# Kernel optimization log

Measured on AMD Instinct MI355X. Metric: run time of the kernel, lower is better.

## Reference

```python
import jax, jax.numpy as jnp
import numpy as np

B = 8192       # number of windows (batch*windows_per_image)
N = 49         # tokens per 7x7 window
C = 128        # channels
H = 4          # heads
HD = C // H    # head dim = 32
WIN = (7, 7)


def _relative_position_index(win):
    wh, ww = win
    coords = np.stack(np.meshgrid(np.arange(wh), np.arange(ww), indexing='ij'))
    cf = coords.reshape(2, -1)                       # (2, N)
    rel = (cf[:, :, None] - cf[:, None, :]).transpose(1, 2, 0)  # (N, N, 2)
    rel[:, :, 0] += wh - 1
    rel[:, :, 1] += ww - 1
    rel[:, :, 0] *= 2 * ww - 1
    return jnp.array(rel.sum(-1).reshape(-1), dtype=jnp.int32)  # (N*N,)


def setup_inputs() -> dict:
    key = jax.random.key(0)
    ks = jax.random.split(key, 7)
    x = jax.random.normal(ks[0], (B, N, C), dtype=jnp.float32)
    mask = jax.random.normal(ks[1], (B, 1, N, N), dtype=jnp.float32)
    qkv_w = jax.random.normal(ks[2], (C, 3 * C), dtype=jnp.float32) * (C ** -0.5)
    qkv_b = jnp.zeros((3 * C,), dtype=jnp.float32)
    rel_bias_table = jax.random.normal(ks[3], ((2 * WIN[0] - 1) * (2 * WIN[1] - 1), H), dtype=jnp.float32)
    proj_w = jax.random.normal(ks[4], (C, C), dtype=jnp.float32) * (C ** -0.5)
    proj_b = jnp.zeros((C,), dtype=jnp.float32)
    rel_index = _relative_position_index(WIN)
    return {"x": x, "mask": mask, "qkv_w": qkv_w, "qkv_b": qkv_b,
            "rel_bias_table": rel_bias_table, "proj_w": proj_w,
            "proj_b": proj_b, "rel_index": rel_index}


def reference(x, mask, qkv_w, qkv_b, rel_bias_table, proj_w, proj_b, rel_index):
    b, n, c = x.shape
    scale = HD ** -0.5
    qkv = (x @ qkv_w + qkv_b).reshape(b, n, 3, H, HD).transpose(2, 0, 3, 1, 4)
    q, k, v = qkv[0] * scale, qkv[1], qkv[2]          # (b, H, n, HD)
    attn = jnp.einsum('bhqd,bhkd->bhqk', q, k)        # (b, H, n, n)
    # gathered relative position bias: (n*n, H) -> (1, H, n, n)
    bias = rel_bias_table[rel_index].reshape(n, n, H).transpose(2, 0, 1)[None]
    attn = jax.nn.softmax(attn + bias + mask, axis=-1)
    out = jnp.einsum('bhqk,bhkd->bhqd', attn, v)       # (b, H, n, HD)
    out = out.transpose(0, 2, 1, 3).reshape(b, n, c)
    return out @ proj_w + proj_b
```

## Files before the change

### kernel.cpp

```cpp
#include <hip/hip_runtime.h>
#include <hip/hip_bf16.h>

using f32x4 = __attribute__((ext_vector_type(4))) float;
using bf16x8 = __attribute__((ext_vector_type(8))) short;

#define DEVI __device__ __forceinline__

DEVI short f2bf(float f) { __hip_bfloat16 h = __float2bfloat16(f); return *reinterpret_cast<short*>(&h); }
DEVI unsigned int pk2(float a, float b) {
    float2 t; t.x = a; t.y = b;
    __hip_bfloat162 h = __float22bfloat162_rn(t);
    return *reinterpret_cast<unsigned int*>(&h);
}
DEVI float bf2f(unsigned short s) { unsigned int u = ((unsigned int)s) << 16; return __uint_as_float(u); }

DEVI void pl32swap(unsigned& a, unsigned& b) { asm("v_permlane32_swap_b32 %0, %1" : "+v"(a), "+v"(b)); }
DEVI void pl16swap(unsigned& a, unsigned& b) { asm("v_permlane16_swap_b32 %0, %1" : "+v"(a), "+v"(b)); }

#define GLOAD_LDS16(gp, lp) \
    __builtin_amdgcn_global_load_lds((const __attribute__((address_space(1))) void*)(gp), \
                                     (__attribute__((address_space(3))) void*)(lp), 16, 0, 0)

constexpr int NB = 8192;
constexpr int NT = 49;
constexpr int CD = 128;
constexpr float SCALE = 0.17677669529663687f;
constexpr float LOG2E = 1.4426950408889634f;

constexpr size_t WS_QKVWT  = 0;
constexpr size_t WS_PROJWT = 98304;
constexpr size_t WS_BIAS   = 131072;

DEVI void div49(unsigned grow, unsigned& bI, unsigned& tI) {
    bI = (unsigned)(((unsigned long long)grow * 2804876602ull) >> 37);
    tI = grow - bI * 49u;
}

DEVI int swz128(int row, int col) { return row * 128 + (col ^ ((row & 7) << 3)); }

__global__ __launch_bounds__(256) void prep_kernel(
    const float* __restrict__ qkv_w, const float* __restrict__ proj_w,
    const float* __restrict__ rbt, const int* __restrict__ rel_index,
    short* __restrict__ qkvwS, short* __restrict__ projwT, unsigned short* __restrict__ biasBf)
{
    int i = blockIdx.x * 256 + threadIdx.x;
    if (i < 384 * 128) {
        int n = i >> 7, j = i & 127;
        int c = n >> 7, r = n & 127;
        qkvwS[c * 16384 + r * 128 + (j ^ ((r & 7) << 3))] = f2bf(qkv_w[j * 384 + n]);
    }
    if (i < 128 * 128) {
        int n = i >> 7, j = i & 127;
        projwT[n * 128 + j] = f2bf(proj_w[j * 128 + n]);
    }
    if (i < 4 * NT * NT) {
        int h = i / (NT * NT); int t = i % (NT * NT);
        int k = t / NT, q = t - k * NT;
        biasBf[i] = (unsigned short)f2bf(rbt[rel_index[q * NT + k] * 4 + h] * LOG2E);
    }
}

__global__ __launch_bounds__(512, 4) void fused_kernel(
    const float* __restrict__ x, const float* __restrict__ mask,
    const float* __restrict__ qkv_b, const short* __restrict__ qkvwS,
    const unsigned short* __restrict__ biasT, const short* __restrict__ projwT,
    const float* __restrict__ proj_b, float* __restrict__ out)
{
    __shared__ __attribute__((aligned(16))) short pool[40960];
    short* qkL = pool;
    short* vS  = pool + 16384;
    char*  Wcb = (char*)(pool + 24576);
    float* mT  = (float*)(pool + 24576);

    const int b = blockIdx.x;
    const int tid = threadIdx.x;
    const int w = tid >> 6, lane = tid & 63, lr = lane & 15, lg = lane >> 4;
    const int h = w >> 1, half = w & 1;

    const float* mb_ = mask + (size_t)b * (NT * NT);
    float mreg[5];
#pragma unroll
    for (int ii = 0; ii < 5; ++ii) {
        int i = tid + ii * 512;
        mreg[ii] = (i < NT * NT) ? mb_[i] * LOG2E : 0.f;
    }

    bf16x8 af[2][4];
#pragma unroll
    for (int mf = 0; mf < 2; ++mf) {
        const int row = 32 * (w & 1) + 16 * mf + lr;
        const bool valid = row < NT;
        const float* xrow = x + ((size_t)b * NT + (valid ? row : 0)) * CD;
#pragma unroll
        for (int kt = 0; kt < 4; ++kt) {
            float4 v0 = {0.f,0.f,0.f,0.f}, v1 = {0.f,0.f,0.f,0.f};
            if (valid) {
                const float4* p = reinterpret_cast<const float4*>(xrow + kt * 32 + lg * 8);
                v0 = p[0]; v1 = p[1];
            }
            union { unsigned int u[4]; bf16x8 v; } cv;
            cv.u[0] = pk2(v0.x, v0.y); cv.u[1] = pk2(v0.z, v0.w);
            cv.u[2] = pk2(v1.x, v1.y); cv.u[3] = pk2(v1.z, v1.w);
            af[mf][kt] = cv.v;
        }
    }

    float biasr[3][2];
#pragma unroll
    for (int c = 0; c < 3; ++c)
#pragma unroll
        for (int nn = 0; nn < 2; ++nn)
            biasr[c][nn] = qkv_b[(c * 8 + (w >> 1) + 4 * nn) * 16 + lr];

    const char* srcW = (const char*)qkvwS;
#pragma unroll
    for (int c = 0; c < 3; ++c) {
#pragma unroll
        for (int i = 0; i < 4; ++i)
            GLOAD_LDS16(srcW + c * 32768 + w * 4096 + i * 1024 + lane * 16,
                        Wcb + w * 4096 + i * 1024);
        __syncthreads();

#pragma unroll
        for (int nn = 0; nn < 2; ++nn) {
            const int ntl = (w >> 1) + 4 * nn;
            const int nt  = c * 8 + ntl;
            const int s   = nt >> 3;
            const int hh  = (nt >> 1) & 3;
            const int d0  = (nt & 1) * 16;
            const int d   = d0 + lr;
            const float scl = (s == 0) ? SCALE * LOG2E : 1.0f;
#pragma unroll
            for (int mf = 0; mf < 2; ++mf) {
                const int rt = 2 * (w & 1) + mf;
                f32x4 acc = {0.f, 0.f, 0.f, 0.f};
#pragma unroll
                for (int kt = 0; kt < 4; ++kt) {
                    bf16x8 bb = *reinterpret_cast<const bf16x8*>(
                        Wcb + (ntl * 16 + lr) * 256 + ((kt * 64 + lg * 16) ^ ((lr & 7) << 4)));
                    acc = __builtin_amdgcn_mfma_f32_16x16x32_bf16(af[mf][kt], bb, acc, 0, 0, 0);
                }
#pragma unroll
                for (int r = 0; r < 4; ++r) {
                    const int row = rt * 16 + 4 * lg + r;
                    const short val = f2bf((acc[r] + biasr[c][nn]) * scl);
                    if (s < 2) {
                        const int g0 = s * 4 + (d >> 3);
                        qkL[hh * 4096 + row * 64 + (((g0 ^ (row & 7)) << 3) | (d & 7))] = val;
                    } else {
                        const int a2 = row >> 4, bb2 = row & 15;
                        const int col = (bb2 < 8) ? (a2 * 8 + bb2) : (24 + a2 * 8 + bb2);
                        vS[hh * 2048 + d * 64 + (col ^ ((d & 7) << 3))] = val;
                    }
                }
            }
        }
        __syncthreads();
    }

    const int mt0 = 2 * half;
    bf16x8 qa[2], kb[4], vb[2][2];
#pragma unroll
    for (int i = 0; i < 2; ++i) {
        const int row = 16 * (mt0 + i) + lr;
        qa[i] = *reinterpret_cast<const bf16x8*>(&qkL[h * 4096 + row * 64 + ((lg ^ (row & 7)) << 3)]);
    }
#pragma unroll
    for (int t4 = 0; t4 < 4; ++t4) {
        const int row = 16 * t4 + lr;
        kb[t4] = *reinterpret_cast<const bf16x8*>(&qkL[h * 4096 + row * 64 + (((4 | lg) ^ (row & 7)) << 3)]);
    }
    {
        const short* vSl = vS + h * 2048;
        const int sw8 = (lr & 7) << 3;
#pragma unroll
        for (int nt = 0; nt < 2; ++nt)
#pragma unroll
            for (int blk = 0; blk < 2; ++blk)
                vb[nt][blk] = *reinterpret_cast<const bf16x8*>(
                    &vSl[(16 * nt + lr) * 64 + ((blk * 32 + 8 * lg) ^ sw8)]);
    }
#pragma unroll
    for (int ii = 0; ii < 5; ++ii) {
        int i = tid + ii * 512;
        if (i < NT * NT) {
            unsigned q_, k_;
            div49((unsigned)i, q_, k_);
            mT[k_ * 65 + q_] = mreg[ii];
        }
    }
    __syncthreads();

    const unsigned short* biasTh = biasT + h * (NT * NT);
    float mbb[2][4][4];
#pragma unroll
    for (int mt2 = 0; mt2 < 2; ++mt2) {
        const int qcol = 16 * (mt0 + mt2) + lr;
#pragma unroll
        for (int ct = 0; ct < 4; ++ct)
#pragma unroll
            for (int r = 0; r < 4; ++r) {
                int k = 16 * ct + 4 * lg + r;
                int kc = min(k, 49);
                mbb[mt2][ct][r] = mT[kc * 65 + qcol] + bf2f(biasTh[kc * NT + qcol]);
            }
    }

    f32x4 oacc[2][2];
#pragma unroll
    for (int mt2 = 0; mt2 < 2; ++mt2) { oacc[mt2][0] = f32x4{0,0,0,0}; oacc[mt2][1] = f32x4{0,0,0,0}; }

#pragma unroll
    for (int mt2 = 0; mt2 < 2; ++mt2) {
        f32x4 sacc[4];
#pragma unroll
        for (int ct = 0; ct < 4; ++ct) {
            f32x4 z = {0.f, 0.f, 0.f, 0.f};
            sacc[ct] = __builtin_amdgcn_mfma_f32_16x16x32_bf16(kb[ct], qa[mt2], z, 0, 0, 0);
        }

        float e[4][4];
        float psum = 0.f;
#pragma unroll
        for (int ct = 0; ct < 4; ++ct)
#pragma unroll
            for (int r = 0; r < 4; ++r) {
                float ee = exp2f(sacc[ct][r] + mbb[mt2][ct][r]);
                if (ct == 3) ee = (r == 0 && lg == 0) ? ee : 0.f;
                e[ct][r] = ee;
                psum += ee;
            }
        psum += __shfl_xor(psum, 16);
        psum += __shfl_xor(psum, 32);
        const float inv = 1.0f / psum;

        unsigned A0 = pk2(e[0][0] * inv, e[0][1] * inv);
        unsigned A1 = pk2(e[1][0] * inv, e[1][1] * inv);
        unsigned A2 = pk2(e[2][0] * inv, e[2][1] * inv);
        unsigned A3 = pk2(e[3][0] * inv, e[3][1] * inv);
        unsigned B0 = pk2(e[0][2] * inv, e[0][3] * inv);
        unsigned B1 = pk2(e[1][2] * inv, e[1][3] * inv);
        unsigned B2 = pk2(e[2][2] * inv, e[2][3] * inv);
        unsigned B3 = pk2(e[3][2] * inv, e[3][3] * inv);
        pl32swap(A0, A2); pl32swap(A1, A3);
        pl16swap(A0, A1); pl16swap(A2, A3);
        pl32swap(B0, B2); pl32swap(B1, B3);
        pl16swap(B0, B1); pl16swap(B2, B3);
        union { unsigned u[4]; bf16x8 v; } p0, p1;
        p0.u[0] = A0; p0.u[1] = B0; p0.u[2] = A1; p0.u[3] = B1;
        p1.u[0] = A2; p1.u[1] = B2; p1.u[2] = A3; p1.u[3] = B3;

#pragma unroll
        for (int nt = 0; nt < 2; ++nt) {
            oacc[mt2][nt] = __builtin_amdgcn_mfma_f32_16x16x32_bf16(p0.v, vb[nt][0], oacc[mt2][nt], 0, 0, 0);
            oacc[mt2][nt] = __builtin_amdgcn_mfma_f32_16x16x32_bf16(p1.v, vb[nt][1], oacc[mt2][nt], 0, 0, 0);
        }
    }

    short* oS = qkL;
#pragma unroll
    for (int mt2 = 0; mt2 < 2; ++mt2)
#pragma unroll
        for (int nt = 0; nt < 2; ++nt)
#pragma unroll
            for (int r = 0; r < 4; ++r) {
                int row = 16 * (mt0 + mt2) + 4 * lg + r;
                int col = 32 * h + 16 * nt + lr;
                oS[swz128(row, col)] = f2bf(oacc[mt2][nt][r]);
            }
    __syncthreads();

    {
        bf16x8 bbf[4];
        const short* brow = projwT + (w * 16 + lr) * 128 + lg * 8;
#pragma unroll
        for (int kt = 0; kt < 4; ++kt)
            bbf[kt] = *reinterpret_cast<const bf16x8*>(brow + kt * 32);

        f32x4 acc[4];
#pragma unroll
        for (int mf = 0; mf < 4; ++mf) acc[mf] = f32x4{0.f, 0.f, 0.f, 0.f};

#pragma unroll
        for (int mf = 0; mf < 4; ++mf)
#pragma unroll
            for (int kt = 0; kt < 4; ++kt) {
                bf16x8 a2 = *reinterpret_cast<const bf16x8*>(&oS[swz128(16 * mf + lr, kt * 32 + lg * 8)]);
                acc[mf] = __builtin_amdgcn_mfma_f32_16x16x32_bf16(a2, bbf[kt], acc[mf], 0, 0, 0);
            }

        const int col = w * 16 + lr;
        const float pb = proj_b[col];
#pragma unroll
        for (int mf = 0; mf < 4; ++mf)
#pragma unroll
            for (int r = 0; r < 4; ++r) {
                int row = 16 * mf + 4 * lg + r;
                if (row < NT)
                    out[((size_t)b * NT + row) * CD + col] = acc[mf][r] + pb;
            }
    }
}

extern "C" void kernel_launch(void* const* d_in, const int* in_sizes, int n_in,
                              void* d_out, int out_size, void* d_ws, size_t ws_size,
                              hipStream_t stream) {
    const float* x      = (const float*)d_in[0];
    const float* mask   = (const float*)d_in[1];
    const float* qkv_w  = (const float*)d_in[2];
    const float* qkv_b  = (const float*)d_in[3];
    const float* rbt    = (const float*)d_in[4];
    const float* proj_w = (const float*)d_in[5];
    const float* proj_b = (const float*)d_in[6];
    const int*   ridx   = (const int*)d_in[7];
    float* out = (float*)d_out;

    char* ws = (char*)d_ws;
    short* qkvwS  = (short*)(ws + WS_QKVWT);
    short* projwT = (short*)(ws + WS_PROJWT);
    unsigned short* biasBf = (unsigned short*)(ws + WS_BIAS);

    prep_kernel<<<192, 256, 0, stream>>>(qkv_w, proj_w, rbt, ridx, qkvwS, projwT, biasBf);
    fused_kernel<<<NB, 512, 0, stream>>>(x, mask, qkv_b, qkvwS, biasBf, projwT, proj_b, out);
}
```

Measured before the change: 296.7 us.

## Read QKV weights directly from global and shrink LDS to raise occupancy

Drops the staging of QKV weight chunks into LDS through global_load_lds with per-chunk barriers. Each wave now loads its weight fragments straight from global (L2-resident) and computes transposed tiles so Q/K can be written as packed 8-byte stores. LDS drops from 80KB to 48KB and launch bounds rise to 6 blocks per CU. V fragments are loaded lazily inside the PV loop and the mask/bias sums are computed per mt2 to cut register pressure. The cost is more global/L2 weight traffic per block and an extra barrier, since mT now aliases the Q/K region.

```diff
diff --git a/kernel.cpp b/kernel.cpp
--- a/kernel.cpp
+++ b/kernel.cpp
@@ -17,10 +17,6 @@
 DEVI void pl32swap(unsigned& a, unsigned& b) { asm("v_permlane32_swap_b32 %0, %1" : "+v"(a), "+v"(b)); }
 DEVI void pl16swap(unsigned& a, unsigned& b) { asm("v_permlane16_swap_b32 %0, %1" : "+v"(a), "+v"(b)); }
 
-#define GLOAD_LDS16(gp, lp) \
-    __builtin_amdgcn_global_load_lds((const __attribute__((address_space(1))) void*)(gp), \
-                                     (__attribute__((address_space(3))) void*)(lp), 16, 0, 0)
-
 constexpr int NB = 8192;
 constexpr int NT = 49;
 constexpr int CD = 128;
@@ -41,13 +37,12 @@
 __global__ __launch_bounds__(256) void prep_kernel(
     const float* __restrict__ qkv_w, const float* __restrict__ proj_w,
     const float* __restrict__ rbt, const int* __restrict__ rel_index,
-    short* __restrict__ qkvwS, short* __restrict__ projwT, unsigned short* __restrict__ biasBf)
+    short* __restrict__ qkvwT, short* __restrict__ projwT, unsigned short* __restrict__ biasBf)
 {
     int i = blockIdx.x * 256 + threadIdx.x;
     if (i < 384 * 128) {
         int n = i >> 7, j = i & 127;
-        int c = n >> 7, r = n & 127;
-        qkvwS[c * 16384 + r * 128 + (j ^ ((r & 7) << 3))] = f2bf(qkv_w[j * 384 + n]);
+        qkvwT[n * 128 + j] = f2bf(qkv_w[j * 384 + n]);
     }
     if (i < 128 * 128) {
         int n = i >> 7, j = i & 127;
@@ -60,22 +55,24 @@
     }
 }
 
-__global__ __launch_bounds__(512, 4) void fused_kernel(
+__global__ __launch_bounds__(512, 6) void fused_kernel(
     const float* __restrict__ x, const float* __restrict__ mask,
-    const float* __restrict__ qkv_b, const short* __restrict__ qkvwS,
+    const float* __restrict__ qkv_b, const short* __restrict__ qkvwT,
     const unsigned short* __restrict__ biasT, const short* __restrict__ projwT,
     const float* __restrict__ proj_b, float* __restrict__ out)
 {
-    __shared__ __attribute__((aligned(16))) short pool[40960];
-    short* qkL = pool;
-    short* vS  = pool + 16384;
-    char*  Wcb = (char*)(pool + 24576);
-    float* mT  = (float*)(pool + 24576);
+    __shared__ __attribute__((aligned(16))) short pool[24576];
+    char*  qkb = (char*)pool;
+    char*  vSb = (char*)pool + 32768;
+    float* mT  = (float*)pool;
+    short* oS  = pool + 8192;
 
     const int b = blockIdx.x;
     const int tid = threadIdx.x;
     const int w = tid >> 6, lane = tid & 63, lr = lane & 15, lg = lane >> 4;
     const int h = w >> 1, half = w & 1;
+    const int wpair = w >> 1;
+    const int tsel = w & 1;
 
     const float* mb_ = mask + (size_t)b * (NT * NT);
     float mreg[5];
@@ -88,7 +85,7 @@
     bf16x8 af[2][4];
 #pragma unroll
     for (int mf = 0; mf < 2; ++mf) {
-        const int row = 32 * (w & 1) + 16 * mf + lr;
+        const int row = 32 * tsel + 16 * mf + lr;
         const bool valid = row < NT;
         const float* xrow = x + ((size_t)b * NT + (valid ? row : 0)) * CD;
 #pragma unroll
@@ -105,81 +102,80 @@
         }
     }
 
-    float biasr[3][2];
-#pragma unroll
-    for (int c = 0; c < 3; ++c)
-#pragma unroll
-        for (int nn = 0; nn < 2; ++nn)
-            biasr[c][nn] = qkv_b[(c * 8 + (w >> 1) + 4 * nn) * 16 + lr];
-
-    const char* srcW = (const char*)qkvwS;
-#pragma unroll
-    for (int c = 0; c < 3; ++c) {
-#pragma unroll
-        for (int i = 0; i < 4; ++i)
-            GLOAD_LDS16(srcW + c * 32768 + w * 4096 + i * 1024 + lane * 16,
-                        Wcb + w * 4096 + i * 1024);
-        __syncthreads();
-
+#pragma unroll
+    for (int c = 0; c < 2; ++c) {
 #pragma unroll
         for (int nn = 0; nn < 2; ++nn) {
-            const int ntl = (w >> 1) + 4 * nn;
-            const int nt  = c * 8 + ntl;
-            const int s   = nt >> 3;
-            const int hh  = (nt >> 1) & 3;
-            const int d0  = (nt & 1) * 16;
-            const int d   = d0 + lr;
-            const float scl = (s == 0) ? SCALE * LOG2E : 1.0f;
-#pragma unroll
-            for (int mf = 0; mf < 2; ++mf) {
-                const int rt = 2 * (w & 1) + mf;
+            const int ntl = wpair + 4 * nn;
+            const int nt = c * 8 + ntl;
+            const int hh = (ntl >> 1) & 3;
+            const int dtile = ntl & 1;
+            bf16x8 wf[4];
+            const short* wr_ = qkvwT + (nt * 16 + lr) * 128 + lg * 8;
+#pragma unroll
+            for (int kt = 0; kt < 4; ++kt)
+                wf[kt] = *reinterpret_cast<const bf16x8*>(wr_ + kt * 32);
+            const float4 b4 = *reinterpret_cast<const float4*>(qkv_b + nt * 16 + 4 * lg);
+            const float scl = (c == 0) ? SCALE * LOG2E : 1.0f;
+#pragma unroll
+            for (int tf = 0; tf < 2; ++tf) {
                 f32x4 acc = {0.f, 0.f, 0.f, 0.f};
 #pragma unroll
-                for (int kt = 0; kt < 4; ++kt) {
-                    bf16x8 bb = *reinterpret_cast<const bf16x8*>(
-                        Wcb + (ntl * 16 + lr) * 256 + ((kt * 64 + lg * 16) ^ ((lr & 7) << 4)));
-                    acc = __builtin_amdgcn_mfma_f32_16x16x32_bf16(af[mf][kt], bb, acc, 0, 0, 0);
-                }
-#pragma unroll
-                for (int r = 0; r < 4; ++r) {
-                    const int row = rt * 16 + 4 * lg + r;
-                    const short val = f2bf((acc[r] + biasr[c][nn]) * scl);
-                    if (s < 2) {
-                        const int g0 = s * 4 + (d >> 3);
-                        qkL[hh * 4096 + row * 64 + (((g0 ^ (row & 7)) << 3) | (d & 7))] = val;
-                    } else {
-                        const int a2 = row >> 4, bb2 = row & 15;
-                        const int col = (bb2 < 8) ? (a2 * 8 + bb2) : (24 + a2 * 8 + bb2);
-                        vS[hh * 2048 + d * 64 + (col ^ ((d & 7) << 3))] = val;
-                    }
-                }
-            }
-        }
-        __syncthreads();
-    }
+                for (int kt = 0; kt < 4; ++kt)
+                    acc = __builtin_amdgcn_mfma_f32_16x16x32_bf16(wf[kt], af[tf][kt], acc, 0, 0, 0);
+                const int t = 16 * (2 * tsel + tf) + lr;
+                const int gp = (dtile * 4 + lg) ^ (t & 6);
+                uint2 s;
+                s.x = pk2((acc[0] + b4.x) * scl, (acc[1] + b4.y) * scl);
+                s.y = pk2((acc[2] + b4.z) * scl, (acc[3] + b4.w) * scl);
+                *reinterpret_cast<uint2*>(qkb + c * 16384 + hh * 4096 + t * 64 + gp * 8) = s;
+            }
+        }
+    }
+#pragma unroll
+    for (int nn = 0; nn < 2; ++nn) {
+        const int ntl = wpair + 4 * nn;
+        const int nt = 16 + ntl;
+        const int hh = (ntl >> 1) & 3;
+        const int d0 = (ntl & 1) * 16;
+        bf16x8 wf[4];
+        const short* wr_ = qkvwT + (nt * 16 + lr) * 128 + lg * 8;
+#pragma unroll
+        for (int kt = 0; kt < 4; ++kt)
+            wf[kt] = *reinterpret_cast<const bf16x8*>(wr_ + kt * 32);
+        const float bv = qkv_b[nt * 16 + lr];
+        const int d = d0 + lr;
+#pragma unroll
+        for (int tf = 0; tf < 2; ++tf) {
+            f32x4 acc = {0.f, 0.f, 0.f, 0.f};
+#pragma unroll
+            for (int kt = 0; kt < 4; ++kt)
+                acc = __builtin_amdgcn_mfma_f32_16x16x32_bf16(af[tf][kt], wf[kt], acc, 0, 0, 0);
+            const int tt = 2 * tsel + tf;
+            const int slotq = (lg < 2) ? (tt * 8 + 4 * lg) : (24 + tt * 8 + 4 * lg);
+            const int gp = (slotq >> 2) ^ ((d & 7) << 1);
+            uint2 s;
+            s.x = pk2(acc[0] + bv, acc[1] + bv);
+            s.y = pk2(acc[2] + bv, acc[3] + bv);
+            *reinterpret_cast<uint2*>(vSb + hh * 4096 + d * 128 + gp * 8) = s;
+        }
+    }
+    __syncthreads();
 
     const int mt0 = 2 * half;
-    bf16x8 qa[2], kb[4], vb[2][2];
+    bf16x8 qa[2], kb[4];
 #pragma unroll
     for (int i = 0; i < 2; ++i) {
-        const int row = 16 * (mt0 + i) + lr;
-        qa[i] = *reinterpret_cast<const bf16x8*>(&qkL[h * 4096 + row * 64 + ((lg ^ (row & 7)) << 3)]);
+        const int t = 16 * (mt0 + i) + lr;
+        qa[i] = *reinterpret_cast<const bf16x8*>(qkb + h * 4096 + t * 64 + ((16 * lg) ^ ((t & 6) << 3)));
     }
 #pragma unroll
     for (int t4 = 0; t4 < 4; ++t4) {
-        const int row = 16 * t4 + lr;
-        kb[t4] = *reinterpret_cast<const bf16x8*>(&qkL[h * 4096 + row * 64 + (((4 | lg) ^ (row & 7)) << 3)]);
-    }
-    {
-        const short* vSl = vS + h * 2048;
-        const int sw8 = (lr & 7) << 3;
-#pragma unroll
-        for (int nt = 0; nt < 2; ++nt)
-#pragma unroll
-            for (int blk = 0; blk < 2; ++blk)
-                vb[nt][blk] = *reinterpret_cast<const bf16x8*>(
-                    &vSl[(16 * nt + lr) * 64 + ((blk * 32 + 8 * lg) ^ sw8)]);
-    }
+        const int t = 16 * t4 + lr;
+        kb[t4] = *reinterpret_cast<const bf16x8*>(qkb + 16384 + h * 4096 + t * 64 + ((16 * lg) ^ ((t & 6) << 3)));
+    }
+    __syncthreads();
+
 #pragma unroll
     for (int ii = 0; ii < 5; ++ii) {
         int i = tid + ii * 512;
@@ -192,26 +188,27 @@
     __syncthreads();
 
     const unsigned short* biasTh = biasT + h * (NT * NT);
-    float mbb[2][4][4];
+    const short* vSs = (short*)vSb + h * 2048;
+    const int sw8 = (lr & 7) << 3;
+
+    f32x4 oacc[2][2];
+#pragma unroll
+    for (int mt2 = 0; mt2 < 2; ++mt2) { oacc[mt2][0] = f32x4{0,0,0,0}; oacc[mt2][1] = f32x4{0,0,0,0}; }
+
 #pragma unroll
     for (int mt2 = 0; mt2 < 2; ++mt2) {
         const int qcol = 16 * (mt0 + mt2) + lr;
+
+        float mbb[4][4];
 #pragma unroll
         for (int ct = 0; ct < 4; ++ct)
 #pragma unroll
             for (int r = 0; r < 4; ++r) {
                 int k = 16 * ct + 4 * lg + r;
                 int kc = min(k, 49);
-                mbb[mt2][ct][r] = mT[kc * 65 + qcol] + bf2f(biasTh[kc * NT + qcol]);
-            }
-    }
-
-    f32x4 oacc[2][2];
-#pragma unroll
-    for (int mt2 = 0; mt2 < 2; ++mt2) { oacc[mt2][0] = f32x4{0,0,0,0}; oacc[mt2][1] = f32x4{0,0,0,0}; }
-
-#pragma unroll
-    for (int mt2 = 0; mt2 < 2; ++mt2) {
+                mbb[ct][r] = mT[kc * 65 + qcol] + bf2f(biasTh[kc * NT + qcol]);
+            }
+
         f32x4 sacc[4];
 #pragma unroll
         for (int ct = 0; ct < 4; ++ct) {
@@ -225,7 +222,7 @@
         for (int ct = 0; ct < 4; ++ct)
 #pragma unroll
             for (int r = 0; r < 4; ++r) {
-                float ee = exp2f(sacc[ct][r] + mbb[mt2][ct][r]);
+                float ee = exp2f(sacc[ct][r] + mbb[ct][r]);
                 if (ct == 3) ee = (r == 0 && lg == 0) ? ee : 0.f;
                 e[ct][r] = ee;
                 psum += ee;
@@ -252,12 +249,13 @@
 
 #pragma unroll
         for (int nt = 0; nt < 2; ++nt) {
-            oacc[mt2][nt] = __builtin_amdgcn_mfma_f32_16x16x32_bf16(p0.v, vb[nt][0], oacc[mt2][nt], 0, 0, 0);
-            oacc[mt2][nt] = __builtin_amdgcn_mfma_f32_16x16x32_bf16(p1.v, vb[nt][1], oacc[mt2][nt], 0, 0, 0);
-        }
-    }
-
-    short* oS = qkL;
+            bf16x8 vb0 = *reinterpret_cast<const bf16x8*>(&vSs[(16 * nt + lr) * 64 + ((8 * lg) ^ sw8)]);
+            bf16x8 vb1 = *reinterpret_cast<const bf16x8*>(&vSs[(16 * nt + lr) * 64 + ((32 + 8 * lg) ^ sw8)]);
+            oacc[mt2][nt] = __builtin_amdgcn_mfma_f32_16x16x32_bf16(p0.v, vb0, oacc[mt2][nt], 0, 0, 0);
+            oacc[mt2][nt] = __builtin_amdgcn_mfma_f32_16x16x32_bf16(p1.v, vb1, oacc[mt2][nt], 0, 0, 0);
+        }
+    }
+
 #pragma unroll
     for (int mt2 = 0; mt2 < 2; ++mt2)
 #pragma unroll
@@ -316,10 +314,10 @@
     float* out = (float*)d_out;
 
     char* ws = (char*)d_ws;
-    short* qkvwS  = (short*)(ws + WS_QKVWT);
+    short* qkvwT  = (short*)(ws + WS_QKVWT);
     short* projwT = (short*)(ws + WS_PROJWT);
     unsigned short* biasBf = (unsigned short*)(ws + WS_BIAS);
 
-    prep_kernel<<<192, 256, 0, stream>>>(qkv_w, proj_w, rbt, ridx, qkvwS, projwT, biasBf);
-    fused_kernel<<<NB, 512, 0, stream>>>(x, mask, qkv_b, qkvwS, biasBf, projwT, proj_b, out);
-}
+    prep_kernel<<<192, 256, 0, stream>>>(qkv_w, proj_w, rbt, ridx, qkvwT, projwT, biasBf);
+    fused_kernel<<<NB, 512, 0, stream>>>(x, mask, qkv_b, qkvwT, biasBf, projwT, proj_b, out);
+}
```

Result: slower. 442.9 us (+49.2%).
